# Kernel tuning notes

Hardware: AMD Instinct MI355X
Metric: run time of the kernel (lower is better)

## Reference

```python
import jax, jax.numpy as jnp
import numpy as np

IN_SHAPE = 4096
H_S = 250        # sender_hidden
H_R = 100        # receiver_hidden
MAX_LEN = 30     # message_shape[0]
VOCAB = 40       # message_shape[1]; EOS = VOCAB-1
OUT_CLS = 512 ** 2  # out_shape[1] ** out_shape[0]


def lstm_cell(x, h, c, W_ih, W_hh, b_ih, b_hh):
    # PyTorch LSTM cell: gate order i, f, g, o
    gates = W_ih @ x + b_ih + W_hh @ h + b_hh
    i, f, g, o = jnp.split(gates, 4)
    c_new = jax.nn.sigmoid(f) * c + jax.nn.sigmoid(i) * jnp.tanh(g)
    h_new = jax.nn.sigmoid(o) * jnp.tanh(c_new)
    return h_new, c_new


def setup_inputs() -> dict:
    key = jax.random.key(0)
    ks = jax.random.split(key, 16)
    s = 0.05
    return {
        "x": jax.random.normal(ks[0], (IN_SHAPE,), dtype=jnp.float32),
        "gumbel_noise": jax.random.gumbel(ks[1], (MAX_LEN, VOCAB), dtype=jnp.float32),
        "W_s1": jax.random.normal(ks[2], (H_S, IN_SHAPE)) * s,
        "b_s1": jnp.zeros((H_S,), jnp.float32),
        "W_ih1": jax.random.normal(ks[3], (4 * H_S, VOCAB)) * s,
        "W_hh1": jax.random.normal(ks[4], (4 * H_S, H_S)) * s,
        "b_ih1": jnp.zeros((4 * H_S,), jnp.float32),
        "b_hh1": jnp.zeros((4 * H_S,), jnp.float32),
        "W_p": jax.random.normal(ks[5], (VOCAB, H_S)) * s,
        "b_p": jnp.zeros((VOCAB,), jnp.float32),
        "W_ih2": jax.random.normal(ks[6], (4 * H_R, VOCAB)) * s,
        "W_hh2": jax.random.normal(ks[7], (4 * H_R, H_R)) * s,
        "b_ih2": jnp.zeros((4 * H_R,), jnp.float32),
        "b_hh2": jnp.zeros((4 * H_R,), jnp.float32),
        "W_r": jax.random.normal(ks[8], (OUT_CLS, H_R)) * s,
        "b_r": jnp.zeros((OUT_CLS,), jnp.float32),
    }


def reference(x, gumbel_noise, W_s1, b_s1, W_ih1, W_hh1, b_ih1, b_hh1,
              W_p, b_p, W_ih2, W_hh2, b_ih2, b_hh2, W_r, b_r):
    dt = x.dtype
    eos = jax.nn.one_hot(VOCAB - 1, VOCAB, dtype=dt)
    # sender: h0 = relu(sender1(x)), c0 = 0, first input = sos = zeros
    h0 = jax.nn.relu(W_s1 @ x + b_s1)
    c0 = jnp.zeros((H_S,), dt)
    sos = jnp.zeros((VOCAB,), dt)
    is_last = jnp.arange(MAX_LEN) == MAX_LEN - 1

    def sender_step(carry, inp):
        h, c, sym, done = carry
        g, last = inp
        nh, nc = lstm_cell(sym, h, c, W_ih1, W_hh1, b_ih1, b_hh1)
        logits = W_p @ nh + b_p
        soft = jax.nn.softmax(logits + g)  # gumbel_softmax, tau=1
        idx = jnp.argmax(soft)
        hard = jax.nn.one_hot(idx, VOCAB, dtype=dt)
        st = hard + soft - jax.lax.stop_gradient(soft)  # straight-through
        # at max length the original appends the plain EOS constant
        emit = jnp.where(last & ~done, eos, st)
        emit = jnp.where(done, eos, emit)
        valid = ~done  # this symbol is part of the message
        new_done = done | (idx == VOCAB - 1) | last
        h = jnp.where(done, h, nh)
        c = jnp.where(done, c, nc)
        sym = jnp.where(done, sym, emit)
        return (h, c, sym, new_done), (emit, valid)

    _, (msg, valid) = jax.lax.scan(
        sender_step, (h0, c0, sos, jnp.array(False)), (gumbel_noise, is_last))

    # receiver LSTM: consume message up to and including first EOS (freeze after)
    def recv_step(carry, inp):
        h, c = carry
        sym, v = inp
        nh, nc = lstm_cell(sym, h, c, W_ih2, W_hh2, b_ih2, b_hh2)
        return (jnp.where(v, nh, h), jnp.where(v, nc, c)), None

    (hR, _), _ = jax.lax.scan(
        recv_step, (jnp.zeros((H_R,), dt), jnp.zeros((H_R,), dt)), (msg, valid))
    return jax.nn.softmax(W_r @ hR + b_r)  # [OUT_CLS]
```

## Files before the change

### kernel.cpp

```cpp
#include <hip/hip_runtime.h>
#include <math.h>

#define HS    250
#define HRr   100
#define VOC   40
#define TMAX  30
#define NCLS  262144
#define KS    10
#define RPB   25
#define GRID  256
#define NOUT  (GRID - KS - 1)
#define NCHUNK (NCLS / 256)

typedef unsigned long long ull;

#define PKNH(wsp, par) ((ull*)(wsp) + (size_t)(par) * 256)
#define PKLP(wsp, par) ((ull*)(wsp) + 512 + (size_t)(par) * 400)
#define PKMSG(wsp)     ((ull*)(wsp) + 1312)
#define PKHR(wsp)      ((ull*)(wsp) + 2596)
#define WS_SUMS 5024
#define WS_ZERO_BYTES 21568

#define AST(p, v) __hip_atomic_store((p), (v), __ATOMIC_RELAXED, __HIP_MEMORY_SCOPE_AGENT)
#define ALD(p)    __hip_atomic_load((p), __ATOMIC_RELAXED, __HIP_MEMORY_SCOPE_AGENT)

__device__ __forceinline__ float sigf(float x) { return 1.f / (1.f + expf(-x)); }
__device__ __forceinline__ float lanebc(float v, int l) {
  return __int_as_float(__builtin_amdgcn_readlane(__float_as_int(v), l));
}
__device__ __forceinline__ ull packtv(unsigned tag, float v) {
  return ((ull)tag << 32) | (ull)__float_as_uint(v);
}
__device__ __forceinline__ float lowf(ull w) { return __uint_as_float((unsigned)w); }

#define SENDER_GATES(P, HV)                                   \
  {                                                           \
    _Pragma("unroll")                                         \
    for (int i = 0; i < 64; i += 4) {                         \
      a0 += whh[i    ] * lanebc(HV, i    );                   \
      a1 += whh[i + 1] * lanebc(HV, i + 1);                   \
      a2 += whh[i + 2] * lanebc(HV, i + 2);                   \
      a3 += whh[i + 3] * lanebc(HV, i + 3);                   \
    }                                                         \
    _Pragma("unroll")                                         \
    for (int i = 0; i < 10; i += 2) {                         \
      a0 += wih[i    ] * lanebc(sv, (P) * 10 + i    );        \
      a1 += wih[i + 1] * lanebc(sv, (P) * 10 + i + 1);        \
    }                                                         \
  }

#define RED(x) ((part[(x)] + part[100 + (x)]) + (part[200 + (x)] + part[300 + (x)]))

__global__ __launch_bounds__(512, 2) void k_mega(
    const float* __restrict__ x,
    const float* __restrict__ W_s1,  const float* __restrict__ b_s1,
    const float* __restrict__ gum,
    const float* __restrict__ W_ih1, const float* __restrict__ W_hh1,
    const float* __restrict__ b_ih1, const float* __restrict__ b_hh1,
    const float* __restrict__ W_p,   const float* __restrict__ b_p,
    const float* __restrict__ W_ih2, const float* __restrict__ W_hh2,
    const float* __restrict__ b_ih2, const float* __restrict__ b_hh2,
    const float* __restrict__ W_r,   const float* __restrict__ b_r,
    float* __restrict__ ws,          float* __restrict__ out) {
  __shared__ float part[400];
  __shared__ float h0L[32];
  __shared__ float hx[256];
  __shared__ float lpx[400];
  __shared__ float symx[VOC];
  __shared__ int   doneL;
  __shared__ float gL[400];
  __shared__ float hL[HRr];
  __shared__ float hfs[HRr];
  __shared__ float4 h4[25];
  __shared__ float  red8[8];

  const int b    = blockIdx.x;
  const int t0   = threadIdx.x;
  const int lane = t0 & 63;
  const int w    = t0 >> 6;

  if (b < KS) {
    const int p    = w & 3;
    const int lr   = ((w >> 2) << 6) + lane;
    const bool gact = (lr < 100);
    const int gi   = lr / 25, rr = lr % 25;
    const int grow = gi * 250 + b * RPB + rr;

    float whh[64], wih[10], bsum = 0.f;
    if (gact) {
      #pragma unroll
      for (int i = 0; i < 64; i++) {
        int k = p * 64 + i;
        whh[i] = (k < HS) ? W_hh1[(size_t)grow * HS + k] : 0.f;
      }
      #pragma unroll
      for (int i = 0; i < 10; i++) wih[i] = W_ih1[grow * VOC + p * 10 + i];
      bsum = b_ih1[grow] + b_hh1[grow];
    }
    float wps[RPB];
    if (w == 0) {
      #pragma unroll
      for (int r = 0; r < RPB; r++)
        wps[r] = (lane < VOC) ? W_p[lane * HS + b * RPB + r] : 0.f;
    }
    const float bpv = (lane < VOC) ? b_p[lane] : 0.f;

    {
      const int nr = (w == 7) ? 4 : 3;
      for (int j = 0; j < nr; ++j) {
        const int r = 3 * w + j;
        const float4* wr = (const float4*)(W_s1 + (size_t)(b * RPB + r) * 4096);
        const float4* xr = (const float4*)x;
        float a0 = 0.f, a1 = 0.f, a2 = 0.f, a3 = 0.f;
        #pragma unroll
        for (int q = 0; q < 16; ++q) {
          float4 w4 = wr[lane + (q << 6)], x4 = xr[lane + (q << 6)];
          a0 += w4.x * x4.x; a1 += w4.y * x4.y; a2 += w4.z * x4.z; a3 += w4.w * x4.w;
        }
        float acc = (a0 + a1) + (a2 + a3);
        #pragma unroll
        for (int o = 32; o; o >>= 1) acc += __shfl_down(acc, o);
        if (lane == 0) h0L[r] = acc + b_s1[b * RPB + r];
      }
    }
    __syncthreads();
    if (w == 0 && lane < RPB) {
      float hn0 = fmaxf(h0L[lane], 0.f);
      AST(&PKNH(ws, 1)[b * RPB + lane], packtv(1u, hn0));
    }

    float c  = 0.f;
    float sv = 0.f;
    const bool h3v = (192 + lane) < HS;
    const bool l6v = lane < (400 - 384);

    for (int s = 0; s <= TMAX; ++s) {
      float gv = 0.f;
      if (s > 0 && lane < VOC) gv = gum[(s - 1) * VOC + lane];

      if (w == 0) {
        const unsigned need = (unsigned)(s + 1);
        const int par = (s + 1) & 1;
        const ull* nhp = PKNH(ws, par);
        const ull* lpp = PKLP(ws, par);
        const bool lpact = (s > 0);
        const ull dummy = (ull)need << 32;
        ull hw0, hw1, hw2, hw3;
        ull lw0 = 0, lw1 = 0, lw2 = 0, lw3 = 0, lw4 = 0, lw5 = 0, lw6 = 0;
        for (;;) {
          hw0 = ALD(&nhp[lane]);
          hw1 = ALD(&nhp[64 + lane]);
          hw2 = ALD(&nhp[128 + lane]);
          hw3 = h3v ? ALD(&nhp[192 + lane]) : dummy;
          bool ok = (unsigned)(hw0 >> 32) == need && (unsigned)(hw1 >> 32) == need &&
                    (unsigned)(hw2 >> 32) == need && (unsigned)(hw3 >> 32) == need;
          if (lpact) {
            lw0 = ALD(&lpp[lane]);        lw1 = ALD(&lpp[64 + lane]);
            lw2 = ALD(&lpp[128 + lane]);  lw3 = ALD(&lpp[192 + lane]);
            lw4 = ALD(&lpp[256 + lane]);  lw5 = ALD(&lpp[320 + lane]);
            lw6 = l6v ? ALD(&lpp[384 + lane]) : dummy;
            ok = ok && (unsigned)(lw0 >> 32) == need && (unsigned)(lw1 >> 32) == need &&
                       (unsigned)(lw2 >> 32) == need && (unsigned)(lw3 >> 32) == need &&
                       (unsigned)(lw4 >> 32) == need && (unsigned)(lw5 >> 32) == need &&
                       (unsigned)(lw6 >> 32) == need;
          }
          if (__all(ok)) break;
        }
        hx[lane] = lowf(hw0); hx[64 + lane] = lowf(hw1); hx[128 + lane] = lowf(hw2);
        if (h3v) hx[192 + lane] = lowf(hw3);
        if (lpact) {
          lpx[lane] = lowf(lw0);        lpx[64 + lane] = lowf(lw1);
          lpx[128 + lane] = lowf(lw2);  lpx[192 + lane] = lowf(lw3);
          lpx[256 + lane] = lowf(lw4);  lpx[320 + lane] = lowf(lw5);
          if (l6v) lpx[384 + lane] = lowf(lw6);
        }
      }
      __syncthreads();

      float hv0 = hx[lane], hv1 = hx[64 + lane], hv2 = hx[128 + lane];
      float hv3 = h3v ? hx[192 + lane] : 0.f;

      if (s > 0) {
        float lg = -INFINITY;
        if (lane < VOC) {
          float acc = bpv + gv;
          #pragma unroll
          for (int m = 0; m < KS; ++m) acc += lpx[m * VOC + lane];
          lg = acc;
        }
        float v = lg; int bi = lane;
        #pragma unroll
        for (int o = 32; o; o >>= 1) {
          float ov = __shfl_down(v, o);
          int   oi = __shfl_down(bi, o);
          if (ov > v) { v = ov; bi = oi; }
        }
        float m  = __shfl(v, 0);
        int  idx = __shfl(bi, 0);
        float e = (lane < VOC) ? expf(lg - m) : 0.f;
        float ssum = e;
        #pragma unroll
        for (int o = 32; o; o >>= 1) ssum += __shfl_down(ssum, o);
        ssum = __shfl(ssum, 0);
        float soft = e / ssum;
        float hard = (lane == idx) ? 1.f : 0.f;
        float st   = (hard + soft) - soft;
        const bool last = (s - 1 == TMAX - 1);
        float emit = last ? ((lane == VOC - 1) ? 1.f : 0.f) : st;
        const bool done = (idx == VOC - 1) || last;
        if (b == 0 && w == 0 && lane < VOC)
          AST(&PKMSG(ws)[(s - 1) * VOC + lane],
              packtv((unsigned)s | (done ? 0x10000u : 0u), emit));
        sv = (lane < VOC) ? emit : 0.f;
        if (done) break;
      }

      if (gact) {
        float a0 = bsum, a1 = 0.f, a2 = 0.f, a3 = 0.f;
        if      (p == 0) SENDER_GATES(0, hv0)
        else if (p == 1) SENDER_GATES(1, hv1)
        else if (p == 2) SENDER_GATES(2, hv2)
        else             SENDER_GATES(3, hv3)
        part[p * 100 + lr] = (a0 + a1) + (a2 + a3);
      }
      __syncthreads();

      if (w == 0) {
        float gi_ = RED(lane < RPB ? lane : 0);
        float gf_ = RED(25 + (lane < RPB ? lane : 0));
        float gg_ = RED(50 + (lane < RPB ? lane : 0));
        float go_ = RED(75 + (lane < RPB ? lane : 0));
        float ig = sigf(gi_), fg = sigf(gf_), gg = tanhf(gg_), og = sigf(go_);
        float cn = fg * c + ig * gg; c = cn;
        float hn = og * tanhf(cn);
        float lpsum = 0.f;
        #pragma unroll
        for (int r = 0; r < RPB; ++r) lpsum += wps[r] * lanebc(hn, r);
        const unsigned nt = (unsigned)(s + 2);
        const int np = (s + 2) & 1;
        if (lane < RPB) AST(&PKNH(ws, np)[b * RPB + lane], packtv(nt, hn));
        if (lane < VOC) AST(&PKLP(ws, np)[b * VOC + lane], packtv(nt, lpsum));
      }
    }
  } else if (b == KS) {
    const bool act = (t0 < 400);
    float wih2[VOC], whh2[HRr], bsum2 = 0.f;
    if (act) {
      #pragma unroll
      for (int i = 0; i < VOC; i++) wih2[i] = W_ih2[t0 * VOC + i];
      #pragma unroll
      for (int i = 0; i < HRr; i++) whh2[i] = W_hh2[t0 * HRr + i];
      bsum2 = b_ih2[t0] + b_hh2[t0];
    }
    float c2 = 0.f, rv0 = 0.f, rv1 = 0.f;

    for (int t = 0; t < TMAX; ++t) {
      if (w == 0) {
        const bool mv = (lane < VOC);
        ull mw = 0;
        for (;;) {
          if (mv) mw = ALD(&PKMSG(ws)[t * VOC + lane]);
          bool ok = !mv || ((unsigned)(mw >> 32) & 0xFFFFu) == (unsigned)(t + 1);
          if (__all(ok)) break;
        }
        if (mv) symx[lane] = lowf(mw);
        if (lane == 0) doneL = (int)(((unsigned)(mw >> 32)) >> 16);
      }
      __syncthreads();
      const bool done = (doneL != 0);
      float sv2 = (lane < VOC) ? symx[lane] : 0.f;
      if (act) {
        float a0 = bsum2, a1 = 0.f, a2 = 0.f, a3 = 0.f;
        #pragma unroll
        for (int i = 0; i < VOC; i += 4) {
          a0 += wih2[i    ] * lanebc(sv2, i    );
          a1 += wih2[i + 1] * lanebc(sv2, i + 1);
          a2 += wih2[i + 2] * lanebc(sv2, i + 2);
          a3 += wih2[i + 3] * lanebc(sv2, i + 3);
        }
        #pragma unroll
        for (int i = 0; i < 64; i += 4) {
          a0 += whh2[i    ] * lanebc(rv0, i    );
          a1 += whh2[i + 1] * lanebc(rv0, i + 1);
          a2 += whh2[i + 2] * lanebc(rv0, i + 2);
          a3 += whh2[i + 3] * lanebc(rv0, i + 3);
        }
        #pragma unroll
        for (int i = 0; i < 36; i += 4) {
          a0 += whh2[64 + i    ] * lanebc(rv1, i    );
          a1 += whh2[64 + i + 1] * lanebc(rv1, i + 1);
          a2 += whh2[64 + i + 2] * lanebc(rv1, i + 2);
          a3 += whh2[64 + i + 3] * lanebc(rv1, i + 3);
        }
        gL[t0] = (a0 + a1) + (a2 + a3);
      }
      __syncthreads();
      if (t0 < HRr) {
        float ig = sigf(gL[t0]);
        float fg = sigf(gL[100 + t0]);
        float gg = tanhf(gL[200 + t0]);
        float og = sigf(gL[300 + t0]);
        float cn = fg * c2 + ig * gg; c2 = cn;
        hL[t0] = og * tanhf(cn);
      }
      __syncthreads();
      rv0 = hL[lane];
      rv1 = (lane < 36) ? hL[64 + lane] : 0.f;
      if (done) break;
    }
    if (t0 < HRr) AST(&PKHR(ws)[t0], packtv(1u, hL[t0]));
  } else {
    const int o = b - KS - 1;
    float dummy = 0.f;
    const float4* wr4 = (const float4*)W_r;
    for (int c = o; c < NCHUNK; c += NOUT) {
      const int f0 = c * 6400;
      for (int i = f0 + t0; i < f0 + 6400; i += 512) {
        float4 w4 = wr4[i];
        dummy += (w4.x + w4.y) + (w4.z + w4.w);
      }
    }
    asm volatile("" :: "v"(dummy));

    if (t0 < HRr) {
      ull hw;
      for (;;) {
        hw = ALD(&PKHR(ws)[t0]);
        if ((unsigned)(hw >> 32) == 1u) break;
        __builtin_amdgcn_s_sleep(64);
      }
      hfs[t0] = lowf(hw);
    }
    __syncthreads();
    if (t0 < 25)
      h4[t0] = make_float4(hfs[4*t0], hfs[4*t0+1], hfs[4*t0+2], hfs[4*t0+3]);
    __syncthreads();

    const int sub = t0 >> 8;
    const int tl  = t0 & 255;
    const int wv  = tl >> 6;
    const int sl  = lane & 31;
    const int hf  = lane >> 5;
    float accs = 0.f;
    for (int c = o; c < NCHUNK; c += NOUT) {
      const int base = c * 256 + sub * 128 + wv * 32;
      #pragma unroll 4
      for (int i = 0; i < 16; ++i) {
        const int row = base + 2 * i + hf;
        float v = 0.f;
        if (sl < 25) {
          float4 w4 = wr4[(size_t)row * 25 + sl];
          float4 hq = h4[sl];
          v = w4.x * hq.x + w4.y * hq.y + w4.z * hq.z + w4.w * hq.w;
        }
        #pragma unroll
        for (int off = 16; off; off >>= 1) v += __shfl_down(v, off, 32);
        float e = 0.f;
        if (sl == 0) { e = expf(v + b_r[row]); accs += e; }
        float eB = __shfl(e, 32);
        if (lane == 0) ((float2*)out)[(base + 2 * i) >> 1] = make_float2(e, eB);
      }
    }
    accs += __shfl_down(accs, 32);
    if (lane == 0) red8[w] = accs;
    __syncthreads();
    if (t0 == 0)
      atomicAdd(&ws[WS_SUMS + (b & 63)],
                ((red8[0] + red8[1]) + (red8[2] + red8[3])) +
                ((red8[4] + red8[5]) + (red8[6] + red8[7])));
  }
}

__global__ __launch_bounds__(256) void k_scale(const float* __restrict__ ws,
                                               float* __restrict__ out) {
  float s = ws[WS_SUMS + (threadIdx.x & 63)];
  #pragma unroll
  for (int o = 1; o < 64; o <<= 1) s += __shfl_xor(s, o);
  const float rinv = 1.f / s;
  const int i = blockIdx.x * 256 + threadIdx.x;
  float4 e = ((const float4*)out)[i];
  e.x *= rinv; e.y *= rinv; e.z *= rinv; e.w *= rinv;
  ((float4*)out)[i] = e;
}

extern "C" void kernel_launch(void* const* d_in, const int* in_sizes, int n_in,
                              void* d_out, int out_size, void* d_ws, size_t ws_size,
                              hipStream_t stream) {
  const float* x     = (const float*)d_in[0];
  const float* gum   = (const float*)d_in[1];
  const float* W_s1  = (const float*)d_in[2];
  const float* b_s1  = (const float*)d_in[3];
  const float* W_ih1 = (const float*)d_in[4];
  const float* W_hh1 = (const float*)d_in[5];
  const float* b_ih1 = (const float*)d_in[6];
  const float* b_hh1 = (const float*)d_in[7];
  const float* W_p   = (const float*)d_in[8];
  const float* b_p   = (const float*)d_in[9];
  const float* W_ih2 = (const float*)d_in[10];
  const float* W_hh2 = (const float*)d_in[11];
  const float* b_ih2 = (const float*)d_in[12];
  const float* b_hh2 = (const float*)d_in[13];
  const float* W_r   = (const float*)d_in[14];
  const float* b_r   = (const float*)d_in[15];
  float* ws  = (float*)d_ws;
  float* out = (float*)d_out;

  (void)hipMemsetAsync(d_ws, 0, WS_ZERO_BYTES, stream);
  k_mega <<<GRID, 512, 0, stream>>>(x, W_s1, b_s1, gum, W_ih1, W_hh1,
                                    b_ih1, b_hh1, W_p, b_p,
                                    W_ih2, W_hh2, b_ih2, b_hh2,
                                    W_r, b_r, ws, out);
  k_scale<<<NCLS/1024, 256, 0, stream>>>(ws, out);
}
```

Before: 346.9 us.

## Fuse softmax normalization into mega kernel via grid barrier, use 1024-thread blocks

Removes the separate k_scale launch. The output blocks now count themselves into a global done counter, spin until all of them have finished, and then each rescales its own output chunks by the reciprocal of the summed exponentials. Blocks grow from 512 to 1024 threads and each output chunk doubles to 512 rows, so each block streams more of W_r per pass. This saves a kernel launch and one extra pass over the output, but adds a spin barrier. That barrier needs every output block to be resident at once. The 1024-thread launch bound may also cap per-thread registers and cause spills in the sender path, which keeps 64 weights per thread in registers.

```diff
diff --git a/kernel.cpp b/kernel.cpp
--- a/kernel.cpp
+++ b/kernel.cpp
@@ -10,7 +10,8 @@
 #define RPB   25
 #define GRID  256
 #define NOUT  (GRID - KS - 1)
-#define NCHUNK (NCLS / 256)
+#define CHROWS 512
+#define NCHUNK (NCLS / CHROWS)
 
 typedef unsigned long long ull;
 
@@ -19,7 +20,8 @@
 #define PKMSG(wsp)     ((ull*)(wsp) + 1312)
 #define PKHR(wsp)      ((ull*)(wsp) + 2596)
 #define WS_SUMS 5024
-#define WS_ZERO_BYTES 21568
+#define CTRL_DONE(wsp) ((unsigned*)((char*)(wsp) + 21568))
+#define WS_ZERO_BYTES 21572
 
 #define AST(p, v) __hip_atomic_store((p), (v), __ATOMIC_RELAXED, __HIP_MEMORY_SCOPE_AGENT)
 #define ALD(p)    __hip_atomic_load((p), __ATOMIC_RELAXED, __HIP_MEMORY_SCOPE_AGENT)
@@ -51,7 +53,7 @@
 
 #define RED(x) ((part[(x)] + part[100 + (x)]) + (part[200 + (x)] + part[300 + (x)]))
 
-__global__ __launch_bounds__(512, 2) void k_mega(
+__global__ __launch_bounds__(1024) void k_mega(
     const float* __restrict__ x,
     const float* __restrict__ W_s1,  const float* __restrict__ b_s1,
     const float* __restrict__ gum,
@@ -72,7 +74,7 @@
   __shared__ float hL[HRr];
   __shared__ float hfs[HRr];
   __shared__ float4 h4[25];
-  __shared__ float  red8[8];
+  __shared__ float  red16[16];
 
   const int b    = blockIdx.x;
   const int t0   = threadIdx.x;
@@ -82,7 +84,7 @@
   if (b < KS) {
     const int p    = w & 3;
     const int lr   = ((w >> 2) << 6) + lane;
-    const bool gact = (lr < 100);
+    const bool gact = (lr < 100) && (w < 8);
     const int gi   = lr / 25, rr = lr % 25;
     const int grow = gi * 250 + b * RPB + rr;
 
@@ -105,7 +107,7 @@
     }
     const float bpv = (lane < VOC) ? b_p[lane] : 0.f;
 
-    {
+    if (w < 8) {
       const int nr = (w == 7) ? 4 : 3;
       for (int j = 0; j < nr; ++j) {
         const int r = 3 * w + j;
@@ -314,8 +316,8 @@
     float dummy = 0.f;
     const float4* wr4 = (const float4*)W_r;
     for (int c = o; c < NCHUNK; c += NOUT) {
-      const int f0 = c * 6400;
-      for (int i = f0 + t0; i < f0 + 6400; i += 512) {
+      const int f0 = c * (CHROWS * 25);
+      for (int i = f0 + t0; i < f0 + CHROWS * 25; i += 1024) {
         float4 w4 = wr4[i];
         dummy += (w4.x + w4.y) + (w4.z + w4.w);
       }
@@ -327,7 +329,7 @@
       for (;;) {
         hw = ALD(&PKHR(ws)[t0]);
         if ((unsigned)(hw >> 32) == 1u) break;
-        __builtin_amdgcn_s_sleep(64);
+        __builtin_amdgcn_s_sleep(128);
       }
       hfs[t0] = lowf(hw);
     }
@@ -343,7 +345,7 @@
     const int hf  = lane >> 5;
     float accs = 0.f;
     for (int c = o; c < NCHUNK; c += NOUT) {
-      const int base = c * 256 + sub * 128 + wv * 32;
+      const int base = c * CHROWS + sub * 128 + wv * 32;
       #pragma unroll 4
       for (int i = 0; i < 16; ++i) {
         const int row = base + 2 * i + hf;
@@ -362,25 +364,35 @@
       }
     }
     accs += __shfl_down(accs, 32);
-    if (lane == 0) red8[w] = accs;
+    if (lane == 0) red16[w] = accs;
     __syncthreads();
-    if (t0 == 0)
-      atomicAdd(&ws[WS_SUMS + (b & 63)],
-                ((red8[0] + red8[1]) + (red8[2] + red8[3])) +
-                ((red8[4] + red8[5]) + (red8[6] + red8[7])));
+    if (t0 == 0) {
+      float tot = (((red16[0] + red16[1]) + (red16[2] + red16[3])) +
+                   ((red16[4] + red16[5]) + (red16[6] + red16[7]))) +
+                  (((red16[8] + red16[9]) + (red16[10] + red16[11])) +
+                   ((red16[12] + red16[13]) + (red16[14] + red16[15])));
+      atomicAdd(&ws[WS_SUMS + (b & 63)], tot);
+      __hip_atomic_fetch_add(CTRL_DONE(ws), 1u, __ATOMIC_RELEASE,
+                             __HIP_MEMORY_SCOPE_AGENT);
+      while (__hip_atomic_load(CTRL_DONE(ws), __ATOMIC_RELAXED,
+                               __HIP_MEMORY_SCOPE_AGENT) < (unsigned)NOUT)
+        __builtin_amdgcn_s_sleep(8);
+    }
+    __syncthreads();
+
+    if (t0 < 128) {
+      float s = __uint_as_float(ALD((const unsigned*)(ws + WS_SUMS) + (lane & 63)));
+      #pragma unroll
+      for (int off = 1; off < 64; off <<= 1) s += __shfl_xor(s, off);
+      const float rinv = 1.f / s;
+      float4* po = (float4*)out;
+      for (int c = o; c < NCHUNK; c += NOUT) {
+        float4 e = po[c * 128 + t0];
+        e.x *= rinv; e.y *= rinv; e.z *= rinv; e.w *= rinv;
+        po[c * 128 + t0] = e;
+      }
+    }
   }
-}
-
-__global__ __launch_bounds__(256) void k_scale(const float* __restrict__ ws,
-                                               float* __restrict__ out) {
-  float s = ws[WS_SUMS + (threadIdx.x & 63)];
-  #pragma unroll
-  for (int o = 1; o < 64; o <<= 1) s += __shfl_xor(s, o);
-  const float rinv = 1.f / s;
-  const int i = blockIdx.x * 256 + threadIdx.x;
-  float4 e = ((const float4*)out)[i];
-  e.x *= rinv; e.y *= rinv; e.z *= rinv; e.w *= rinv;
-  ((float4*)out)[i] = e;
 }
 
 extern "C" void kernel_launch(void* const* d_in, const int* in_sizes, int n_in,
@@ -406,9 +418,8 @@
   float* out = (float*)d_out;
 
   (void)hipMemsetAsync(d_ws, 0, WS_ZERO_BYTES, stream);
-  k_mega <<<GRID, 512, 0, stream>>>(x, W_s1, b_s1, gum, W_ih1, W_hh1,
-                                    b_ih1, b_hh1, W_p, b_p,
-                                    W_ih2, W_hh2, b_ih2, b_hh2,
-                                    W_r, b_r, ws, out);
-  k_scale<<<NCLS/1024, 256, 0, stream>>>(ws, out);
+  k_mega <<<GRID, 1024, 0, stream>>>(x, W_s1, b_s1, gum, W_ih1, W_hh1,
+                                     b_ih1, b_hh1, W_p, b_p,
+                                     W_ih2, W_hh2, b_ih2, b_hh2,
+                                     W_r, b_r, ws, out);
 }
```

Result: slower. 469.0 us (+35.2%).
